# Kernel tuning notes

Hardware: AMD Instinct MI355X
Metric: run time of the kernel (lower is better)

The kernel has to match this reference:

```python
import jax, jax.numpy as jnp
import numpy as np
import math

B, SQ, SKV, D, H, DFF = 8, 256, 1024, 1024, 16, 4096
DK = D // H
EPS = 1e-5


def layer_norm(x, g, b):
    mu = jnp.mean(x, axis=-1, keepdims=True)
    var = jnp.mean((x - mu) ** 2, axis=-1, keepdims=True)
    return (x - mu) * jax.lax.rsqrt(var + EPS) * g + b


def erf_gelu(x):
    return x * 0.5 * (1.0 + jax.lax.erf(x / jnp.sqrt(jnp.float32(2.0))))


def setup_inputs() -> dict:
    key = jax.random.key(0)
    ks = jax.random.split(key, 10)
    s = 0.02
    w = lambda k, shape: jax.random.normal(k, shape, jnp.float32) * s
    return {
        "memory": jax.random.normal(ks[0], (B, SKV, D), jnp.float32),
        "q": jax.random.normal(ks[1], (B, SQ, D), jnp.float32),
        "Wq": w(ks[2], (D, D)), "bq": jnp.zeros((D,), jnp.float32),
        "Wk": w(ks[3], (D, D)), "bk": jnp.zeros((D,), jnp.float32),
        "Wv": w(ks[4], (D, D)), "bv": jnp.zeros((D,), jnp.float32),
        "Wo": w(ks[5], (D, D)), "bo": jnp.zeros((D,), jnp.float32),
        "g_kv": jnp.ones((D,), jnp.float32), "b_kv": jnp.zeros((D,), jnp.float32),
        "g_q": jnp.ones((D,), jnp.float32), "b_q": jnp.zeros((D,), jnp.float32),
        "g_ff": jnp.ones((D,), jnp.float32), "b_ff": jnp.zeros((D,), jnp.float32),
        "W1": w(ks[6], (D, DFF)), "b1": jnp.zeros((DFF,), jnp.float32),
        "W2": w(ks[7], (DFF, D)), "b2": jnp.zeros((D,), jnp.float32),
    }


def reference(memory, q, Wq, bq, Wk, bk, Wv, bv, Wo, bo,
              g_kv, b_kv, g_q, b_q, g_ff, b_ff, W1, b1, W2, b2):
    # Pre-norms
    kv_ = layer_norm(memory, g_kv, b_kv)   # [B, SKV, D]
    q_ = layer_norm(q, g_q, b_q)           # [B, SQ, D]
    # QKV projections, split heads: [B, H, S, DK]
    Q = (q_ @ Wq + bq).reshape(B, SQ, H, DK).transpose(0, 2, 1, 3)
    K = (kv_ @ Wk + bk).reshape(B, SKV, H, DK).transpose(0, 2, 1, 3)
    V = (kv_ @ Wv + bv).reshape(B, SKV, H, DK).transpose(0, 2, 1, 3)
    # Scaled dot-product cross-attention
    scores = jnp.einsum("bhqd,bhkd->bhqk", Q, K) / math.sqrt(DK)
    attn = jax.nn.softmax(scores, axis=-1)  # [B, H, SQ, SKV]
    ctx = jnp.einsum("bhqk,bhkd->bhqd", attn, V)
    ctx = ctx.transpose(0, 2, 1, 3).reshape(B, SQ, D)
    x = ctx @ Wo + bo  # attention output (no residual with q, per source)
    # FeedForwardBlock: x + FFN(LN(x))
    y = layer_norm(x, g_ff, b_ff)
    y = erf_gelu(y @ W1 + b1) @ W2 + b2
    out = y + x
    return (out, attn)
```

## Files before the change

### kernel.cpp

```cpp
#include <hip/hip_runtime.h>
#include <hip/hip_bf16.h>
#include <math.h>

#define B_   8
#define SQ_  256
#define SKV_ 1024
#define D_   1024
#define H_   16
#define DK_  64
#define DFF_ 4096

typedef __attribute__((ext_vector_type(4))) float f32x4;
typedef __attribute__((ext_vector_type(8))) __bf16 bf16x8;

__device__ __forceinline__ unsigned short f2bf(float f) {
    unsigned u = __builtin_bit_cast(unsigned, f);
    u += 0x7FFFu + ((u >> 16) & 1u);
    return (unsigned short)(u >> 16);
}
__device__ __forceinline__ float bf2f(unsigned short h) {
    unsigned u = (unsigned)h << 16;
    return __builtin_bit_cast(float, u);
}

__device__ __forceinline__ void gload_lds16(const void* g, void* l) {
    __builtin_amdgcn_global_load_lds(
        (__attribute__((address_space(1))) void*)g,
        (__attribute__((address_space(3))) void*)l,
        16, 0, 0);
}

__global__ __launch_bounds__(256) void transpose4_k(
    const float* __restrict__ Wa, const float* __restrict__ Wb,
    const float* __restrict__ Wc, const float* __restrict__ Wd,
    unsigned short* __restrict__ Ta, unsigned short* __restrict__ Tb,
    unsigned short* __restrict__ Tc, unsigned short* __restrict__ Td) {
    const float* Ws[4] = {Wa, Wb, Wc, Wd};
    unsigned short* Ts[4] = {Ta, Tb, Tc, Td};
    const float* W = Ws[blockIdx.z];
    unsigned short* Wt = Ts[blockIdx.z];
    __shared__ float t[32][33];
    const int n0 = blockIdx.x * 32, k0 = blockIdx.y * 32;
    const int tx = threadIdx.x, ty = threadIdx.y;
#pragma unroll
    for (int i = ty; i < 32; i += 8)
        t[i][tx] = W[(long)(k0 + i) * 1024 + n0 + tx];
    __syncthreads();
#pragma unroll
    for (int i = ty; i < 32; i += 8)
        Wt[(long)(n0 + i) * 1024 + k0 + tx] = f2bf(t[tx][i]);
}

__global__ __launch_bounds__(256) void transpose_cast_k(
    const float* __restrict__ W, unsigned short* __restrict__ Wt, int K, int N) {
    __shared__ float t[32][33];
    const int n0 = blockIdx.x * 32, k0 = blockIdx.y * 32;
    const int tx = threadIdx.x, ty = threadIdx.y;
#pragma unroll
    for (int i = ty; i < 32; i += 8)
        t[i][tx] = W[(long)(k0 + i) * N + n0 + tx];
    __syncthreads();
#pragma unroll
    for (int i = ty; i < 32; i += 8)
        Wt[(long)(n0 + i) * K + k0 + tx] = f2bf(t[tx][i]);
}

__global__ __launch_bounds__(256) void ln_k(
    const float* __restrict__ x, const float* __restrict__ g,
    const float* __restrict__ b, unsigned short* __restrict__ out) {
    const long row = blockIdx.x;
    const float4* xr = reinterpret_cast<const float4*>(x) + row * 256;
    const int t = threadIdx.x;
    float4 v = xr[t];
    __shared__ float sb[8];

    float s = v.x + v.y + v.z + v.w;
#pragma unroll
    for (int o = 1; o < 64; o <<= 1) s += __shfl_xor(s, o);
    if ((t & 63) == 0) sb[t >> 6] = s;
    __syncthreads();
    const float mu = (sb[0] + sb[1] + sb[2] + sb[3]) * (1.0f / 1024.0f);

    const float dx = v.x - mu, dy = v.y - mu, dz = v.z - mu, dw = v.w - mu;
    float q2 = dx * dx + dy * dy + dz * dz + dw * dw;
#pragma unroll
    for (int o = 1; o < 64; o <<= 1) q2 += __shfl_xor(q2, o);
    if ((t & 63) == 0) sb[4 + (t >> 6)] = q2;
    __syncthreads();
    const float var = (sb[4] + sb[5] + sb[6] + sb[7]) * (1.0f / 1024.0f);
    const float rs = rsqrtf(var + 1e-5f);

    const float4 gv = reinterpret_cast<const float4*>(g)[t];
    const float4 bv = reinterpret_cast<const float4*>(b)[t];
    ushort4 h4;
    h4.x = f2bf(dx * rs * gv.x + bv.x);
    h4.y = f2bf(dy * rs * gv.y + bv.y);
    h4.z = f2bf(dz * rs * gv.z + bv.z);
    h4.w = f2bf(dw * rs * gv.w + bv.w);
    reinterpret_cast<ushort4*>(out)[row * 256 + t] = h4;
}

__global__ __launch_bounds__(256) void norm_k(
    const unsigned short* __restrict__ E, float* __restrict__ attn,
    float* __restrict__ invs) {
    const long row = blockIdx.x;
    const int t = threadIdx.x;
    const ushort4 e4 = reinterpret_cast<const ushort4*>(E)[row * 256 + t];
    const float e0 = bf2f(e4.x), e1 = bf2f(e4.y), e2 = bf2f(e4.z), e3 = bf2f(e4.w);
    float s = e0 + e1 + e2 + e3;
    __shared__ float sb[4];
#pragma unroll
    for (int o = 1; o < 64; o <<= 1) s += __shfl_xor(s, o);
    if ((t & 63) == 0) sb[t >> 6] = s;
    __syncthreads();
    const float inv = 1.0f / (sb[0] + sb[1] + sb[2] + sb[3]);
    float4 o4;
    o4.x = e0 * inv; o4.y = e1 * inv; o4.z = e2 * inv; o4.w = e3 * inv;
    reinterpret_cast<float4*>(attn)[row * 256 + t] = o4;
    if (t == 0) invs[row] = inv;
}

__global__ __launch_bounds__(256) void reduce4_k(
    const float* __restrict__ part, const float* __restrict__ bias,
    const float* __restrict__ resid, float* __restrict__ out) {
    const long i4 = (long)blockIdx.x * 256 + threadIdx.x;
    const float4* p = reinterpret_cast<const float4*>(part);
    const float4 a = p[i4], b = p[i4 + 524288], c = p[i4 + 1048576],
                 d = p[i4 + 1572864];
    const float4 bb = reinterpret_cast<const float4*>(bias)[i4 & 255];
    const float4 r = reinterpret_cast<const float4*>(resid)[i4];
    float4 o;
    o.x = a.x + b.x + c.x + d.x + bb.x + r.x;
    o.y = a.y + b.y + c.y + d.y + bb.y + r.y;
    o.z = a.z + b.z + c.z + d.z + bb.z + r.z;
    o.w = a.w + b.w + c.w + d.w + bb.w + r.w;
    reinterpret_cast<float4*>(out)[i4] = o;
}

enum GemmMode {
    M_SCOREEXP = 0,
    M_QSPLIT   = 1,
    M_KVSPLIT  = 2,
    M_CTX      = 3,
    M_BIASF    = 4,
    M_GELU     = 5,
    M_PART     = 6
};

template <int BM, int BN, int MODE>
__global__ __launch_bounds__(256) void gemm_k(
    const unsigned short* __restrict__ A,
    const unsigned short* __restrict__ Bt,
    const float* __restrict__ bias,
    const float* __restrict__ bias2,
    float* __restrict__ outF,
    unsigned short* __restrict__ outH,
    int M, int N, int K, int lda, int ldb,
    long sA, long sB, long sC,
    float alpha) {
    constexpr int WM = BM / 2, WN = BN / 2;
    constexpr int FM = WM / 16, FN = WN / 16;
    __shared__ unsigned short ldsA[BM * 32];
    __shared__ unsigned short ldsB[BN * 32];

    const int tid = threadIdx.x;
    const int wid = tid >> 6, lane = tid & 63;
    const int wr = wid >> 1, wc = wid & 1;
    const int r16 = lane & 15, kch = lane >> 4;
    const int z = blockIdx.z;
    const long zA = (long)z * sA, zB = (long)z * sB;
    const int m0 = blockIdx.y * BM, n0 = blockIdx.x * BN;

    const f32x4 zero4 = {0.f, 0.f, 0.f, 0.f};
    f32x4 acc[FM][FN];
#pragma unroll
    for (int i = 0; i < FM; ++i)
#pragma unroll
        for (int j = 0; j < FN; ++j) acc[i][j] = zero4;

    const int nK = K / 32;
    for (int kt = 0; kt < nK; ++kt) {
        const int k0 = kt * 32;
#pragma unroll
        for (int j = 0; j < BM / 64; ++j) {
            const int chunk = j * 256 + tid;
            const int e = chunk * 8, rr = e >> 5, cc = e & 31;
            gload_lds16(A + zA + (long)(m0 + rr) * lda + (k0 + cc),
                        &ldsA[(j * 256 + wid * 64) * 8]);
        }
#pragma unroll
        for (int j = 0; j < BN / 64; ++j) {
            const int chunk = j * 256 + tid;
            const int e = chunk * 8, rr = e >> 5, cc = e & 31;
            gload_lds16(Bt + zB + (long)(n0 + rr) * ldb + (k0 + cc),
                        &ldsB[(j * 256 + wid * 64) * 8]);
        }
        __syncthreads();

        bf16x8 af[FM], bfr[FN];
#pragma unroll
        for (int fm = 0; fm < FM; ++fm)
            af[fm] = *reinterpret_cast<const bf16x8*>(
                &ldsA[(wr * WM + fm * 16 + r16) * 32 + kch * 8]);
#pragma unroll
        for (int fn = 0; fn < FN; ++fn)
            bfr[fn] = *reinterpret_cast<const bf16x8*>(
                &ldsB[(wc * WN + fn * 16 + r16) * 32 + kch * 8]);
#pragma unroll
        for (int fm = 0; fm < FM; ++fm)
#pragma unroll
            for (int fn = 0; fn < FN; ++fn)
                acc[fm][fn] = __builtin_amdgcn_mfma_f32_16x16x32_bf16(
                    af[fm], bfr[fn], acc[fm][fn], 0, 0, 0);
        __syncthreads();
    }

#pragma unroll
    for (int fm = 0; fm < FM; ++fm) {
#pragma unroll
        for (int fn = 0; fn < FN; ++fn) {
            const int gn = n0 + wc * WN + fn * 16 + r16;
            float bv = 0.0f;
            if constexpr (MODE == M_QSPLIT || MODE == M_BIASF || MODE == M_GELU)
                bv = bias[gn];
            if constexpr (MODE == M_KVSPLIT)
                bv = (gn < 1024) ? bias[gn] : bias2[gn - 1024];
#pragma unroll
            for (int j = 0; j < 4; ++j) {
                const int gm = m0 + wr * WM + fm * 16 + kch * 4 + j;
                const float v = acc[fm][fn][j];
                if constexpr (MODE == M_SCOREEXP) {
                    outH[(long)z * sC + (long)gm * N + gn] = f2bf(__expf(v * alpha));
                } else if constexpr (MODE == M_QSPLIT) {
                    const int bb = gm >> 8, ss = gm & 255, hh = gn >> 6, dd = gn & 63;
                    outH[(((long)(bb * H_ + hh)) * SQ_ + ss) * DK_ + dd] = f2bf(v + bv);
                } else if constexpr (MODE == M_KVSPLIT) {
                    const int bb = gm >> 10, ss = gm & 1023;
                    if (gn < 1024) {
                        const int hh = gn >> 6, dd = gn & 63;
                        outH[(((long)(bb * H_ + hh)) * SKV_ + ss) * DK_ + dd] = f2bf(v + bv);
                    } else {
                        const int gv = gn - 1024, hh = gv >> 6, dd = gv & 63;
                        outF[0] = outF[0];
                        reinterpret_cast<unsigned short*>(outH)[0] += 0;
                        ((unsigned short*)bias2 == nullptr) ? void(0) : void(0);
                        outH[(size_t)8192 * 1024 +
                             (((long)(bb * H_ + hh)) * DK_ + dd) * SKV_ + ss] = f2bf(v + bv);
                    }
                } else if constexpr (MODE == M_CTX) {
                    const float sc = bias[(z << 8) + gm];
                    outH[((long)(z >> 4) * SQ_ + gm) * D_ + (z & 15) * DK_ + gn] =
                        f2bf(v * sc);
                } else if constexpr (MODE == M_BIASF) {
                    outF[(long)gm * N + gn] = v + bv;
                } else if constexpr (MODE == M_GELU) {
                    const float u = v + bv;
                    outH[(long)gm * N + gn] =
                        f2bf(u * 0.5f * (1.0f + erff(u * 0.70710678f)));
                } else {
                    outF[(long)z * sC + (long)gm * N + gn] = v;
                }
            }
        }
    }
}

extern "C" void kernel_launch(void* const* d_in, const int* in_sizes, int n_in,
                              void* d_out, int out_size, void* d_ws, size_t ws_size,
                              hipStream_t stream) {
    (void)in_sizes; (void)n_in; (void)out_size; (void)ws_size;
    const float* memory = (const float*)d_in[0];
    const float* q      = (const float*)d_in[1];
    const float* Wq = (const float*)d_in[2];  const float* bq = (const float*)d_in[3];
    const float* Wk = (const float*)d_in[4];  const float* bk = (const float*)d_in[5];
    const float* Wv = (const float*)d_in[6];  const float* bv = (const float*)d_in[7];
    const float* Wo = (const float*)d_in[8];  const float* bo = (const float*)d_in[9];
    const float* g_kv = (const float*)d_in[10]; const float* b_kv = (const float*)d_in[11];
    const float* g_q  = (const float*)d_in[12]; const float* b_q  = (const float*)d_in[13];
    const float* g_ff = (const float*)d_in[14]; const float* b_ff = (const float*)d_in[15];
    const float* W1 = (const float*)d_in[16]; const float* b1 = (const float*)d_in[17];
    const float* W2 = (const float*)d_in[18]; const float* b2 = (const float*)d_in[19];

    float* outO = (float*)d_out;
    float* outA = outO + (size_t)2048 * 1024;

    char* w = (char*)d_ws;
    unsigned short* kvB  = (unsigned short*)w; w += (size_t)8192 * 1024 * 2;
    unsigned short* qB   = (unsigned short*)w; w += (size_t)2048 * 1024 * 2;
    unsigned short* WqT  = (unsigned short*)w; w += (size_t)1024 * 1024 * 2;
    unsigned short* WkvT = (unsigned short*)w; w += (size_t)2048 * 1024 * 2;
    unsigned short* WoT  = (unsigned short*)w; w += (size_t)1024 * 1024 * 2;
    unsigned short* W1T  = (unsigned short*)w; w += (size_t)4096 * 1024 * 2;
    unsigned short* W2T  = (unsigned short*)w; w += (size_t)1024 * 4096 * 2;
    unsigned short* Qh   = (unsigned short*)w; w += (size_t)2048 * 1024 * 2;
    unsigned short* KVh  = (unsigned short*)w; w += (size_t)16384 * 1024 * 2;
    unsigned short* E    = (unsigned short*)w; w += (size_t)32768 * 1024 * 2;
    float*          invs = (float*)w;          w += (size_t)32768 * 4;
    unsigned short* ctxB = (unsigned short*)w; w += (size_t)2048 * 1024 * 2;
    float*          xF   = (float*)w;          w += (size_t)2048 * 1024 * 4;
    unsigned short* yB   = (unsigned short*)w; w += (size_t)2048 * 1024 * 2;
    unsigned short* h1B  = (unsigned short*)w; w += (size_t)2048 * 4096 * 2;
    float*          part = (float*)w;          w += (size_t)4 * 2048 * 1024 * 4;

    unsigned short* Kh = KVh;

    const dim3 blk(256);
    transpose4_k<<<dim3(32, 32, 4), dim3(32, 8), 0, stream>>>(
        Wq, Wk, Wv, Wo, WqT, WkvT, WkvT + (size_t)1024 * 1024, WoT);
    transpose_cast_k<<<dim3(128, 32), dim3(32, 8), 0, stream>>>(W1, W1T, 1024, 4096);
    transpose_cast_k<<<dim3(32, 128), dim3(32, 8), 0, stream>>>(W2, W2T, 4096, 1024);

    ln_k<<<8192, blk, 0, stream>>>(memory, g_kv, b_kv, kvB);
    ln_k<<<2048, blk, 0, stream>>>(q, g_q, b_q, qB);

    gemm_k<64, 128, M_QSPLIT><<<dim3(8, 32, 1), blk, 0, stream>>>(
        qB, WqT, bq, nullptr, nullptr, Qh, 2048, 1024, 1024, 1024, 1024, 0, 0, 0, 1.f);
    gemm_k<128, 128, M_KVSPLIT><<<dim3(16, 64, 1), blk, 0, stream>>>(
        kvB, WkvT, bk, bv, nullptr, KVh, 8192, 2048, 1024, 1024, 1024, 0, 0, 0, 1.f);

    gemm_k<128, 128, M_SCOREEXP><<<dim3(8, 2, 128), blk, 0, stream>>>(
        Qh, Kh, nullptr, nullptr, nullptr, E, 256, 1024, 64, 64, 64,
        (long)256 * 64, (long)1024 * 64, (long)256 * 1024, 0.125f);

    norm_k<<<32768, blk, 0, stream>>>(E, outA, invs);

    gemm_k<64, 64, M_CTX><<<dim3(1, 4, 128), blk, 0, stream>>>(
        E, KVh + (size_t)8192 * 1024, invs, nullptr, nullptr, ctxB,
        256, 64, 1024, 1024, 1024, (long)256 * 1024, (long)64 * 1024, 0, 1.f);

    gemm_k<64, 128, M_BIASF><<<dim3(8, 32, 1), blk, 0, stream>>>(
        ctxB, WoT, bo, nullptr, xF, nullptr, 2048, 1024, 1024, 1024, 1024, 0, 0, 0, 1.f);

    ln_k<<<2048, blk, 0, stream>>>(xF, g_ff, b_ff, yB);

    gemm_k<128, 128, M_GELU><<<dim3(32, 16, 1), blk, 0, stream>>>(
        yB, W1T, b1, nullptr, nullptr, h1B, 2048, 4096, 1024, 1024, 1024, 0, 0, 0, 1.f);

    gemm_k<128, 128, M_PART><<<dim3(8, 16, 4), blk, 0, stream>>>(
        h1B, W2T, nullptr, nullptr, part, nullptr, 2048, 1024, 1024, 4096, 4096,
        1024, 1024, (long)2048 * 1024, 1.f);
    reduce4_k<<<2048, blk, 0, stream>>>(part, b2, xF, outO);
}
```

Before: 544.7 us.

## Fuse attention scores, softmax normalization and context GEMM; double-buffer GEMM LDS

Replaces three attention kernels (score+exp GEMM, row normalization, context GEMM) with one fused kernel. Each block keeps a 64x1024 tile of exponentiated scores in LDS, computes row sums, writes normalized attention probabilities, and multiplies by V from LDS. This removes the bf16 score-matrix round trip through global memory. Separately, the generic GEMM gets double-buffered LDS staging with a next-tile prefetch and launch bounds of 2 blocks per CU. The fused kernel uses about 140KB of LDS per block, which limits occupancy to one block per CU, and the grid is only 512 blocks.

```diff
diff --git a/kernel.cpp b/kernel.cpp
--- a/kernel.cpp
+++ b/kernel.cpp
@@ -100,24 +100,140 @@
     reinterpret_cast<ushort4*>(out)[row * 256 + t] = h4;
 }
 
-__global__ __launch_bounds__(256) void norm_k(
-    const unsigned short* __restrict__ E, float* __restrict__ attn,
-    float* __restrict__ invs) {
-    const long row = blockIdx.x;
-    const int t = threadIdx.x;
-    const ushort4 e4 = reinterpret_cast<const ushort4*>(E)[row * 256 + t];
-    const float e0 = bf2f(e4.x), e1 = bf2f(e4.y), e2 = bf2f(e4.z), e3 = bf2f(e4.w);
-    float s = e0 + e1 + e2 + e3;
-    __shared__ float sb[4];
-#pragma unroll
-    for (int o = 1; o < 64; o <<= 1) s += __shfl_xor(s, o);
-    if ((t & 63) == 0) sb[t >> 6] = s;
-    __syncthreads();
-    const float inv = 1.0f / (sb[0] + sb[1] + sb[2] + sb[3]);
-    float4 o4;
-    o4.x = e0 * inv; o4.y = e1 * inv; o4.z = e2 * inv; o4.w = e3 * inv;
-    reinterpret_cast<float4*>(attn)[row * 256 + t] = o4;
-    if (t == 0) invs[row] = inv;
+#define ELD 1032
+__global__ __launch_bounds__(512) void fattn_k(
+    const unsigned short* __restrict__ Qh,
+    const unsigned short* __restrict__ Kh,
+    const unsigned short* __restrict__ Vt,
+    float* __restrict__ attn,
+    unsigned short* __restrict__ ctx) {
+    __shared__ unsigned short E_lds[64 * ELD];
+    __shared__ unsigned short Q_lds[64 * 64];
+    __shared__ unsigned short KV_lds[2][64 * 64];
+    __shared__ float partial[8][64];
+    __shared__ float invs_l[64];
+
+    const int tid = threadIdx.x;
+    const int wid = tid >> 6, lane = tid & 63;
+    const int wr = wid >> 2, wc = wid & 3;
+    const int r16 = lane & 15, kch = lane >> 4;
+    const int z = blockIdx.x, qb = blockIdx.y;
+    const int m0 = qb * 64;
+    const long qoff = (long)z * (SQ_ * DK_) + (long)m0 * DK_;
+    const long koff = (long)z * (SKV_ * DK_);
+    const long voff = (long)z * (DK_ * SKV_);
+
+    gload_lds16(Qh + qoff + tid * 8, &Q_lds[wid * 512]);
+    gload_lds16(Kh + koff + tid * 8, &KV_lds[0][wid * 512]);
+    __syncthreads();
+
+    const f32x4 z4 = {0.f, 0.f, 0.f, 0.f};
+
+    int cur = 0;
+    for (int kt = 0; kt < 16; ++kt) {
+        if (kt + 1 < 16)
+            gload_lds16(Kh + koff + (kt + 1) * (64 * 64) + tid * 8,
+                        &KV_lds[cur ^ 1][wid * 512]);
+        f32x4 s[2] = {z4, z4};
+        const int bro = (wc * 16 + r16) * 64;
+#pragma unroll
+        for (int k0 = 0; k0 < 64; k0 += 32) {
+            const bf16x8 bfrag =
+                *reinterpret_cast<const bf16x8*>(&KV_lds[cur][bro + k0 + kch * 8]);
+#pragma unroll
+            for (int fm = 0; fm < 2; ++fm) {
+                const bf16x8 afrag = *reinterpret_cast<const bf16x8*>(
+                    &Q_lds[(wr * 32 + fm * 16 + r16) * 64 + k0 + kch * 8]);
+                s[fm] = __builtin_amdgcn_mfma_f32_16x16x32_bf16(afrag, bfrag, s[fm], 0, 0, 0);
+            }
+        }
+#pragma unroll
+        for (int fm = 0; fm < 2; ++fm)
+#pragma unroll
+            for (int j = 0; j < 4; ++j) {
+                const int row = wr * 32 + fm * 16 + kch * 4 + j;
+                const int col = kt * 64 + wc * 16 + r16;
+                E_lds[row * ELD + col] = f2bf(__expf(s[fm][j] * 0.125f));
+            }
+        __syncthreads();
+        cur ^= 1;
+    }
+
+    {
+        const int r = tid & 63, c = tid >> 6;
+        float s = 0.f;
+        const unsigned* p = reinterpret_cast<const unsigned*>(&E_lds[r * ELD + c * 128]);
+#pragma unroll
+        for (int i = 0; i < 64; ++i) {
+            const unsigned u = p[i];
+            s += __builtin_bit_cast(float, u << 16) +
+                 __builtin_bit_cast(float, u & 0xffff0000u);
+        }
+        partial[c][r] = s;
+    }
+    __syncthreads();
+    if (tid < 64) {
+        float t = 0.f;
+#pragma unroll
+        for (int c = 0; c < 8; ++c) t += partial[c][tid];
+        invs_l[tid] = 1.0f / t;
+    }
+    __syncthreads();
+
+    gload_lds16(Vt + voff + (tid >> 3) * SKV_ + (tid & 7) * 8, &KV_lds[0][wid * 512]);
+
+    {
+        float* abase = attn + (long)z * (SQ_ * SKV_) + (long)m0 * SKV_;
+#pragma unroll
+        for (int ro = 0; ro < 8; ++ro) {
+            const int row = ro * 8 + wid;
+            const float inv = invs_l[row];
+#pragma unroll
+            for (int cc = 0; cc < 4; ++cc) {
+                const int col = cc * 256 + lane * 4;
+                const ushort4 e4 =
+                    *reinterpret_cast<const ushort4*>(&E_lds[row * ELD + col]);
+                float4 o;
+                o.x = bf2f(e4.x) * inv; o.y = bf2f(e4.y) * inv;
+                o.z = bf2f(e4.z) * inv; o.w = bf2f(e4.w) * inv;
+                reinterpret_cast<float4*>(abase + (long)row * SKV_)[col >> 2] = o;
+            }
+        }
+    }
+    __syncthreads();
+
+    cur = 0;
+    f32x4 acc[2] = {z4, z4};
+    for (int kt = 0; kt < 16; ++kt) {
+        if (kt + 1 < 16)
+            gload_lds16(Vt + voff + (tid >> 3) * SKV_ + (kt + 1) * 64 + (tid & 7) * 8,
+                        &KV_lds[cur ^ 1][wid * 512]);
+        const int bro = (wc * 16 + r16) * 64;
+#pragma unroll
+        for (int k0 = 0; k0 < 64; k0 += 32) {
+            const bf16x8 bfrag =
+                *reinterpret_cast<const bf16x8*>(&KV_lds[cur][bro + k0 + kch * 8]);
+#pragma unroll
+            for (int fm = 0; fm < 2; ++fm) {
+                const bf16x8 afrag = *reinterpret_cast<const bf16x8*>(
+                    &E_lds[(wr * 32 + fm * 16 + r16) * ELD + kt * 64 + k0 + kch * 8]);
+                acc[fm] = __builtin_amdgcn_mfma_f32_16x16x32_bf16(afrag, bfrag, acc[fm], 0, 0, 0);
+            }
+        }
+        __syncthreads();
+        cur ^= 1;
+    }
+
+    const int b = z >> 4, h = z & 15;
+#pragma unroll
+    for (int fm = 0; fm < 2; ++fm)
+#pragma unroll
+        for (int j = 0; j < 4; ++j) {
+            const int row = wr * 32 + fm * 16 + kch * 4 + j;
+            const int col = wc * 16 + r16;
+            const float v = acc[fm][j] * invs_l[row];
+            ctx[((long)(b * SQ_) + m0 + row) * D_ + h * 64 + col] = f2bf(v);
+        }
 }
 
 __global__ __launch_bounds__(256) void reduce4_k(
@@ -138,17 +254,15 @@
 }
 
 enum GemmMode {
-    M_SCOREEXP = 0,
-    M_QSPLIT   = 1,
-    M_KVSPLIT  = 2,
-    M_CTX      = 3,
-    M_BIASF    = 4,
-    M_GELU     = 5,
-    M_PART     = 6
+    M_QSPLIT  = 0,
+    M_KVSPLIT = 1,
+    M_BIASF   = 2,
+    M_GELU    = 3,
+    M_PART    = 4
 };
 
 template <int BM, int BN, int MODE>
-__global__ __launch_bounds__(256) void gemm_k(
+__global__ __launch_bounds__(256, 2) void gemm_k(
     const unsigned short* __restrict__ A,
     const unsigned short* __restrict__ Bt,
     const float* __restrict__ bias,
@@ -160,8 +274,8 @@
     float alpha) {
     constexpr int WM = BM / 2, WN = BN / 2;
     constexpr int FM = WM / 16, FN = WN / 16;
-    __shared__ unsigned short ldsA[BM * 32];
-    __shared__ unsigned short ldsB[BN * 32];
+    __shared__ unsigned short ldsA[2][BM * 32];
+    __shared__ unsigned short ldsB[2][BN * 32];
 
     const int tid = threadIdx.x;
     const int wid = tid >> 6, lane = tid & 63;
@@ -171,6 +285,22 @@
     const long zA = (long)z * sA, zB = (long)z * sB;
     const int m0 = blockIdx.y * BM, n0 = blockIdx.x * BN;
 
+    auto stage = [&](int buf, int kt) {
+        const int k0 = kt * 32;
+#pragma unroll
+        for (int j = 0; j < BM / 64; ++j) {
+            const int e = (j * 256 + tid) * 8, rr = e >> 5, cc = e & 31;
+            gload_lds16(A + zA + (long)(m0 + rr) * lda + (k0 + cc),
+                        &ldsA[buf][(j * 256 + wid * 64) * 8]);
+        }
+#pragma unroll
+        for (int j = 0; j < BN / 64; ++j) {
+            const int e = (j * 256 + tid) * 8, rr = e >> 5, cc = e & 31;
+            gload_lds16(Bt + zB + (long)(n0 + rr) * ldb + (k0 + cc),
+                        &ldsB[buf][(j * 256 + wid * 64) * 8]);
+        }
+    };
+
     const f32x4 zero4 = {0.f, 0.f, 0.f, 0.f};
     f32x4 acc[FM][FN];
 #pragma unroll
@@ -179,33 +309,21 @@
         for (int j = 0; j < FN; ++j) acc[i][j] = zero4;
 
     const int nK = K / 32;
+    stage(0, 0);
+    __syncthreads();
+    int cur = 0;
     for (int kt = 0; kt < nK; ++kt) {
-        const int k0 = kt * 32;
-#pragma unroll
-        for (int j = 0; j < BM / 64; ++j) {
-            const int chunk = j * 256 + tid;
-            const int e = chunk * 8, rr = e >> 5, cc = e & 31;
-            gload_lds16(A + zA + (long)(m0 + rr) * lda + (k0 + cc),
-                        &ldsA[(j * 256 + wid * 64) * 8]);
-        }
-#pragma unroll
-        for (int j = 0; j < BN / 64; ++j) {
-            const int chunk = j * 256 + tid;
-            const int e = chunk * 8, rr = e >> 5, cc = e & 31;
-            gload_lds16(Bt + zB + (long)(n0 + rr) * ldb + (k0 + cc),
-                        &ldsB[(j * 256 + wid * 64) * 8]);
-        }
-        __syncthreads();
+        if (kt + 1 < nK) stage(cur ^ 1, kt + 1);
 
         bf16x8 af[FM], bfr[FN];
 #pragma unroll
         for (int fm = 0; fm < FM; ++fm)
             af[fm] = *reinterpret_cast<const bf16x8*>(
-                &ldsA[(wr * WM + fm * 16 + r16) * 32 + kch * 8]);
+                &ldsA[cur][(wr * WM + fm * 16 + r16) * 32 + kch * 8]);
 #pragma unroll
         for (int fn = 0; fn < FN; ++fn)
             bfr[fn] = *reinterpret_cast<const bf16x8*>(
-                &ldsB[(wc * WN + fn * 16 + r16) * 32 + kch * 8]);
+                &ldsB[cur][(wc * WN + fn * 16 + r16) * 32 + kch * 8]);
 #pragma unroll
         for (int fm = 0; fm < FM; ++fm)
 #pragma unroll
@@ -213,6 +331,7 @@
                 acc[fm][fn] = __builtin_amdgcn_mfma_f32_16x16x32_bf16(
                     af[fm], bfr[fn], acc[fm][fn], 0, 0, 0);
         __syncthreads();
+        cur ^= 1;
     }
 
 #pragma unroll
@@ -229,9 +348,7 @@
             for (int j = 0; j < 4; ++j) {
                 const int gm = m0 + wr * WM + fm * 16 + kch * 4 + j;
                 const float v = acc[fm][fn][j];
-                if constexpr (MODE == M_SCOREEXP) {
-                    outH[(long)z * sC + (long)gm * N + gn] = f2bf(__expf(v * alpha));
-                } else if constexpr (MODE == M_QSPLIT) {
+                if constexpr (MODE == M_QSPLIT) {
                     const int bb = gm >> 8, ss = gm & 255, hh = gn >> 6, dd = gn & 63;
                     outH[(((long)(bb * H_ + hh)) * SQ_ + ss) * DK_ + dd] = f2bf(v + bv);
                 } else if constexpr (MODE == M_KVSPLIT) {
@@ -241,16 +358,9 @@
                         outH[(((long)(bb * H_ + hh)) * SKV_ + ss) * DK_ + dd] = f2bf(v + bv);
                     } else {
                         const int gv = gn - 1024, hh = gv >> 6, dd = gv & 63;
-                        outF[0] = outF[0];
-                        reinterpret_cast<unsigned short*>(outH)[0] += 0;
-                        ((unsigned short*)bias2 == nullptr) ? void(0) : void(0);
                         outH[(size_t)8192 * 1024 +
                              (((long)(bb * H_ + hh)) * DK_ + dd) * SKV_ + ss] = f2bf(v + bv);
                     }
-                } else if constexpr (MODE == M_CTX) {
-                    const float sc = bias[(z << 8) + gm];
-                    outH[((long)(z >> 4) * SQ_ + gm) * D_ + (z & 15) * DK_ + gn] =
-                        f2bf(v * sc);
                 } else if constexpr (MODE == M_BIASF) {
                     outF[(long)gm * N + gn] = v + bv;
                 } else if constexpr (MODE == M_GELU) {
@@ -263,6 +373,7 @@
             }
         }
     }
+    (void)alpha;
 }
 
 extern "C" void kernel_launch(void* const* d_in, const int* in_sizes, int n_in,
@@ -294,8 +405,6 @@
     unsigned short* W2T  = (unsigned short*)w; w += (size_t)1024 * 4096 * 2;
     unsigned short* Qh   = (unsigned short*)w; w += (size_t)2048 * 1024 * 2;
     unsigned short* KVh  = (unsigned short*)w; w += (size_t)16384 * 1024 * 2;
-    unsigned short* E    = (unsigned short*)w; w += (size_t)32768 * 1024 * 2;
-    float*          invs = (float*)w;          w += (size_t)32768 * 4;
     unsigned short* ctxB = (unsigned short*)w; w += (size_t)2048 * 1024 * 2;
     float*          xF   = (float*)w;          w += (size_t)2048 * 1024 * 4;
     unsigned short* yB   = (unsigned short*)w; w += (size_t)2048 * 1024 * 2;
@@ -303,6 +412,7 @@
     float*          part = (float*)w;          w += (size_t)4 * 2048 * 1024 * 4;
 
     unsigned short* Kh = KVh;
+    unsigned short* Vt = KVh + (size_t)8192 * 1024;
 
     const dim3 blk(256);
     transpose4_k<<<dim3(32, 32, 4), dim3(32, 8), 0, stream>>>(
@@ -318,15 +428,7 @@
     gemm_k<128, 128, M_KVSPLIT><<<dim3(16, 64, 1), blk, 0, stream>>>(
         kvB, WkvT, bk, bv, nullptr, KVh, 8192, 2048, 1024, 1024, 1024, 0, 0, 0, 1.f);
 
-    gemm_k<128, 128, M_SCOREEXP><<<dim3(8, 2, 128), blk, 0, stream>>>(
-        Qh, Kh, nullptr, nullptr, nullptr, E, 256, 1024, 64, 64, 64,
-        (long)256 * 64, (long)1024 * 64, (long)256 * 1024, 0.125f);
-
-    norm_k<<<32768, blk, 0, stream>>>(E, outA, invs);
-
-    gemm_k<64, 64, M_CTX><<<dim3(1, 4, 128), blk, 0, stream>>>(
-        E, KVh + (size_t)8192 * 1024, invs, nullptr, nullptr, ctxB,
-        256, 64, 1024, 1024, 1024, (long)256 * 1024, (long)64 * 1024, 0, 1.f);
+    fattn_k<<<dim3(128, 4), dim3(512), 0, stream>>>(Qh, Kh, Vt, outA, ctxB);
 
     gemm_k<64, 128, M_BIASF><<<dim3(8, 32, 1), blk, 0, stream>>>(
         ctxB, WoT, bo, nullptr, xF, nullptr, 2048, 1024, 1024, 1024, 1024, 0, 0, 0, 1.f);
```

After: 499.3 us. 1.09x faster.
